# Kernel optimization log

Measured on AMD Instinct MI355X. Metric: run time of the kernel, lower is better.

Reference implementation:

```python
import jax, jax.numpy as jnp
import numpy as np

DIM_IN = 1024
DIM_OUT = 1024
B = 8192


def setup_inputs() -> dict:
    key = jax.random.key(0)
    ks = jax.random.split(key, 8)
    d = DIM_IN + DIM_OUT
    bound = 1.0 / np.sqrt(d)
    def lin(kw, kb):
        W = jax.random.uniform(kw, (d, DIM_OUT), jnp.float32, -bound, bound)
        b = jax.random.uniform(kb, (DIM_OUT,), jnp.float32, -bound, bound)
        return W, b
    kx, kh, kc, kp = ks[0], ks[1], ks[2], ks[3]
    pw = jax.random.split(kp, 8)
    W_I, b_I = lin(pw[0], pw[1])
    W_F, b_F = lin(pw[2], pw[3])
    W_G, b_G = lin(pw[4], pw[5])
    W_O, b_O = lin(pw[6], pw[7])
    return {
        "x": jax.random.normal(kx, (B, DIM_IN), jnp.float32),
        "h": jax.random.normal(kh, (B, DIM_OUT), jnp.float32),
        "c": jax.random.normal(kc, (B, DIM_OUT), jnp.float32),
        "W_I": W_I, "b_I": b_I,
        "W_F": W_F, "b_F": b_F,
        "W_G": W_G, "b_G": b_G,
        "W_O": W_O, "b_O": b_O,
    }


def reference(x, h, c, W_I, b_I, W_F, b_F, W_G, b_G, W_O, b_O):
    X = jnp.concatenate([x, h], axis=-1)  # [B, dimIn+dimOut]
    # Fuse the 4 gate projections into one GEMM: [B,d] @ [d, 4*dimOut]
    W = jnp.concatenate([W_I, W_F, W_G, W_O], axis=1)
    b = jnp.concatenate([b_I, b_F, b_G, b_O], axis=0)
    gates = X @ W + b
    i_, f_, g_, o_ = jnp.split(gates, 4, axis=-1)
    I = jax.nn.sigmoid(i_)
    F = jax.nn.sigmoid(f_)
    G = jnp.tanh(g_)
    O = jax.nn.sigmoid(o_)
    C = F * c + I * G
    return O * jnp.tanh(C), C
```

## Files before the change

### kernel.cpp

```cpp
#include <hip/hip_runtime.h>
#include <cstdint>


#define B_ROWS 8192
#define DK 2048
#define DOUT 1024
#define BM 256
#define BN 256
#define BK 64
#define NKT (DK / BK)

typedef __bf16 bf16x8 __attribute__((ext_vector_type(8)));
typedef __bf16 bf16x4 __attribute__((ext_vector_type(4)));
typedef float f32x4 __attribute__((ext_vector_type(4)));

__device__ inline void load16_to_lds(const __bf16* gsrc, __bf16* ldst) {
    __builtin_amdgcn_global_load_lds(
        (const __attribute__((address_space(1))) void*)gsrc,
        (__attribute__((address_space(3))) void*)ldst,
        16, 0, 0);
}

__device__ inline float fast_sigmoid(float x) {
    return __builtin_amdgcn_rcpf(1.0f + __builtin_amdgcn_exp2f(-1.442695041f * x));
}
__device__ inline float fast_tanh(float x) {
    return 1.0f - 2.0f * __builtin_amdgcn_rcpf(1.0f + __builtin_amdgcn_exp2f(2.885390082f * x));
}

__global__ __launch_bounds__(256) void prep_x(const float* __restrict__ x,
                                              const float* __restrict__ h,
                                              __bf16* __restrict__ X) {
    int id = blockIdx.x * 256 + threadIdx.x;
    int b = id >> 9;
    int k = (id & 511) * 4;
    float4 v;
    if (k < 1024) v = *(const float4*)&x[(size_t)b * 1024 + k];
    else          v = *(const float4*)&h[(size_t)b * 1024 + (k - 1024)];
    bf16x4 o = { (__bf16)v.x, (__bf16)v.y, (__bf16)v.z, (__bf16)v.w };
    *(bf16x4*)&X[(size_t)b * 2048 + k] = o;
}

__global__ __launch_bounds__(256) void prep_w(const float* __restrict__ WI,
                                              const float* __restrict__ WF,
                                              const float* __restrict__ WG,
                                              const float* __restrict__ WO,
                                              __bf16* __restrict__ Wt) {
    int kb = blockIdx.x;
    int jb = blockIdx.y;
    int j0 = jb * 32;
    __shared__ float t[32][33];
    int tx = threadIdx.x, ty = threadIdx.y;
    const float* Ws[4] = {WI, WF, WG, WO};
#pragma unroll
    for (int g = 0; g < 4; ++g) {
        const float* W = Ws[g];
#pragma unroll
        for (int yy = 0; yy < 32; yy += 8) {
            int k = kb * 32 + ty + yy;
            t[ty + yy][tx] = W[(size_t)k * 1024 + j0 + tx];
        }
        __syncthreads();
#pragma unroll
        for (int yy = 0; yy < 32; yy += 8) {
            int r = ty + yy;
            int npp = (jb * 2 + (r >> 4)) * 64 + g * 16 + (r & 15);
            Wt[(size_t)npp * 2048 + kb * 32 + tx] = (__bf16)t[tx][r];
        }
        __syncthreads();
    }
}

__global__ __launch_bounds__(512, 2) void lstm_gemm(
    const __bf16* __restrict__ Xbf, const __bf16* __restrict__ Wt,
    const float* __restrict__ c,
    const float* __restrict__ bI, const float* __restrict__ bF,
    const float* __restrict__ bG, const float* __restrict__ bO,
    float* __restrict__ outH, float* __restrict__ outC)
{
    __shared__ __bf16 lds[2][2][2][8192];

    const int tid  = threadIdx.x;
    const int lane = tid & 63;
    const int wave = tid >> 6;
    const int wm = wave >> 2;
    const int wn = wave & 3;

    const int bid = blockIdx.x;
    const int id  = (bid & 7) * 64 + (bid >> 3);
    const int mb = id & 31;
    const int nb = id >> 5;
    const int m0 = mb * BM;
    const int n0 = nb * BN;

    const int o0  = wave * 1024 + lane * 16;
    const int r0  = o0 >> 6;
    const int lc0 = ((o0 >> 4) & 3) ^ ((r0 >> 1) & 3);
    const __bf16* gA0 = Xbf + (size_t)(m0 + r0)       * DK + lc0 * 8;
    const __bf16* gA1 = Xbf + (size_t)(m0 + r0 + 128) * DK + lc0 * 8;
    const __bf16* gB0 = Wt  + (size_t)(n0 + r0)       * DK + lc0 * 8;
    const __bf16* gB1 = Wt  + (size_t)(n0 + r0 + 128) * DK + lc0 * 8;
    const int ls0 = wave * 512;
    const int ls1 = ls0 + 4096;

    const int lr = lane & 15;
    const int pc = (lane >> 4) ^ ((lr >> 1) & 3);
    const int ae = (wm * 128 + lr) * 32 + pc * 8;
    const int be = (wn * 64  + lr) * 32 + pc * 8;

    f32x4 acc[8][4];
#pragma unroll
    for (int i = 0; i < 8; ++i)
#pragma unroll
        for (int g = 0; g < 4; ++g) acc[i][g] = (f32x4){0.f, 0.f, 0.f, 0.f};

#define STAGE_A(d_, kh_, ko_) do { \
    load16_to_lds(gA0 + (ko_) + (kh_) * 32, &lds[d_][0][kh_][ls0]); \
    load16_to_lds(gA1 + (ko_) + (kh_) * 32, &lds[d_][0][kh_][ls1]); } while (0)
#define STAGE_B(d_, kh_, ko_) do { \
    load16_to_lds(gB0 + (ko_) + (kh_) * 32, &lds[d_][1][kh_][ls0]); \
    load16_to_lds(gB1 + (ko_) + (kh_) * 32, &lds[d_][1][kh_][ls1]); } while (0)

    STAGE_A(0, 0, 0);
    STAGE_B(0, 0, 0);
    STAGE_A(0, 1, 0);
    STAGE_B(0, 1, 0);

#pragma unroll 2
    for (int t = 0; t < NKT; ++t) {
        const int d  = t & 1;
        const int dn = d ^ 1;
        const int ko = ((t + 1) & (NKT - 1)) * BK;
#pragma unroll
        for (int kh = 0; kh < 2; ++kh) {
            asm volatile("s_waitcnt vmcnt(4) lgkmcnt(0)" ::: "memory");
            __builtin_amdgcn_s_barrier();
            asm volatile("" ::: "memory");
            bf16x8 a[8], b0, b1;
#pragma unroll
            for (int mi = 0; mi < 8; ++mi)
                a[mi] = *(const bf16x8*)&lds[d][0][kh][ae + mi * 512];
            b0 = *(const bf16x8*)&lds[d][1][kh][be];
            b1 = *(const bf16x8*)&lds[d][1][kh][be + 512];
            STAGE_A(dn, kh, ko);
            __builtin_amdgcn_s_setprio(1);
#pragma unroll
            for (int mi = 0; mi < 8; ++mi) {
                acc[mi][0] = __builtin_amdgcn_mfma_f32_16x16x32_bf16(a[mi], b0, acc[mi][0], 0, 0, 0);
                acc[mi][1] = __builtin_amdgcn_mfma_f32_16x16x32_bf16(a[mi], b1, acc[mi][1], 0, 0, 0);
            }
            __builtin_amdgcn_s_setprio(0);

            asm volatile("s_waitcnt lgkmcnt(0)" ::: "memory");
            __builtin_amdgcn_s_barrier();
            asm volatile("" ::: "memory");
            bf16x8 b2 = *(const bf16x8*)&lds[d][1][kh][be + 1024];
            bf16x8 b3 = *(const bf16x8*)&lds[d][1][kh][be + 1536];
            STAGE_B(dn, kh, ko);
            __builtin_amdgcn_s_setprio(1);
#pragma unroll
            for (int mi = 0; mi < 8; ++mi) {
                acc[mi][2] = __builtin_amdgcn_mfma_f32_16x16x32_bf16(a[mi], b2, acc[mi][2], 0, 0, 0);
                acc[mi][3] = __builtin_amdgcn_mfma_f32_16x16x32_bf16(a[mi], b3, acc[mi][3], 0, 0, 0);
            }
            __builtin_amdgcn_s_setprio(0);
        }
    }
#undef STAGE_A
#undef STAGE_B

    const int col = lane & 15;
    const int j = (nb * 4 + wn) * 16 + col;
    const float biI = bI[j], biF = bF[j], biG = bG[j], biO = bO[j];
    const int rbase = m0 + wm * 128 + ((lane >> 4) << 2);
#pragma unroll
    for (int mi = 0; mi < 8; ++mi) {
#pragma unroll
        for (int r = 0; r < 4; ++r) {
            int row = rbase + mi * 16 + r;
            float I = fast_sigmoid(acc[mi][0][r] + biI);
            float F = fast_sigmoid(acc[mi][1][r] + biF);
            float G = fast_tanh(acc[mi][2][r] + biG);
            float O = fast_sigmoid(acc[mi][3][r] + biO);
            size_t idx = (size_t)row * DOUT + j;
            float Cn = F * c[idx] + I * G;
            outH[idx] = O * fast_tanh(Cn);
            outC[idx] = Cn;
        }
    }
}

extern "C" void kernel_launch(void* const* d_in, const int* in_sizes, int n_in,
                              void* d_out, int out_size, void* d_ws, size_t ws_size,
                              hipStream_t stream) {
    const float* x  = (const float*)d_in[0];
    const float* h  = (const float*)d_in[1];
    const float* c  = (const float*)d_in[2];
    const float* WI = (const float*)d_in[3];
    const float* bI = (const float*)d_in[4];
    const float* WF = (const float*)d_in[5];
    const float* bF = (const float*)d_in[6];
    const float* WG = (const float*)d_in[7];
    const float* bG = (const float*)d_in[8];
    const float* WO = (const float*)d_in[9];
    const float* bO = (const float*)d_in[10];

    __bf16* Xbf = (__bf16*)d_ws;
    __bf16* Wt  = (__bf16*)((char*)d_ws + (size_t)B_ROWS * DK * 2);
    float* outH = (float*)d_out;
    float* outC = outH + (size_t)B_ROWS * DOUT;

    prep_x<<<(B_ROWS * DK / 4) / 256, 256, 0, stream>>>(x, h, Xbf);
    prep_w<<<dim3(DK / 32, DOUT / 32), dim3(32, 8), 0, stream>>>(WI, WF, WG, WO, Wt);
    lstm_gemm<<<dim3((B_ROWS / BM) * (4 * DOUT / BN)), dim3(512), 0, stream>>>(
        Xbf, Wt, c, bI, bF, bG, bO, outH, outC);
}
```

Measured before the change: 311.9 us.

## Switch GEMM to 32x32x16 MFMA with 4x2 wave layout and merge prep kernels

Replaces the 16x16x32 MFMA tiling with 32x32x16 MFMAs. Each wave now owns a 64x128 sub-tile instead of 128x64, which changes the LDS fragment offsets, the weight interleave order, and the epilogue row mapping to match. The K loop is manually unrolled into one load phase per 32-wide K half, with a single barrier instead of two and the A and B prefetches issued together, to cut LDS reads and barrier overhead. The two prep kernels are merged into one launch to remove a kernel launch. The risks are higher register pressure from the 16-wide accumulators and possible LDS bank conflicts in the new access pattern.

After: 312.2 us. About the same (+0.1%).

```diff
diff --git a/kernel.cpp b/kernel.cpp
--- a/kernel.cpp
+++ b/kernel.cpp
@@ -12,7 +12,7 @@
 
 typedef __bf16 bf16x8 __attribute__((ext_vector_type(8)));
 typedef __bf16 bf16x4 __attribute__((ext_vector_type(4)));
-typedef float f32x4 __attribute__((ext_vector_type(4)));
+typedef float f32x16 __attribute__((ext_vector_type(16)));
 
 __device__ inline void load16_to_lds(const __bf16* gsrc, __bf16* ldst) {
     __builtin_amdgcn_global_load_lds(
@@ -28,29 +28,29 @@
     return 1.0f - 2.0f * __builtin_amdgcn_rcpf(1.0f + __builtin_amdgcn_exp2f(2.885390082f * x));
 }
 
-__global__ __launch_bounds__(256) void prep_x(const float* __restrict__ x,
-                                              const float* __restrict__ h,
-                                              __bf16* __restrict__ X) {
-    int id = blockIdx.x * 256 + threadIdx.x;
-    int b = id >> 9;
-    int k = (id & 511) * 4;
-    float4 v;
-    if (k < 1024) v = *(const float4*)&x[(size_t)b * 1024 + k];
-    else          v = *(const float4*)&h[(size_t)b * 1024 + (k - 1024)];
-    bf16x4 o = { (__bf16)v.x, (__bf16)v.y, (__bf16)v.z, (__bf16)v.w };
-    *(bf16x4*)&X[(size_t)b * 2048 + k] = o;
-}
-
-__global__ __launch_bounds__(256) void prep_w(const float* __restrict__ WI,
-                                              const float* __restrict__ WF,
-                                              const float* __restrict__ WG,
-                                              const float* __restrict__ WO,
-                                              __bf16* __restrict__ Wt) {
-    int kb = blockIdx.x;
-    int jb = blockIdx.y;
+__global__ __launch_bounds__(256) void prep_all(
+    const float* __restrict__ x, const float* __restrict__ h,
+    __bf16* __restrict__ X,
+    const float* __restrict__ WI, const float* __restrict__ WF,
+    const float* __restrict__ WG, const float* __restrict__ WO,
+    __bf16* __restrict__ Wt)
+{
+    __shared__ float t[32][33];
+    if (blockIdx.x >= 2048) {
+        int id = (blockIdx.x - 2048) * 256 + threadIdx.x;
+        int b = id >> 9;
+        int k = (id & 511) * 4;
+        float4 v;
+        if (k < 1024) v = *(const float4*)&x[(size_t)b * 1024 + k];
+        else          v = *(const float4*)&h[(size_t)b * 1024 + (k - 1024)];
+        bf16x4 o = { (__bf16)v.x, (__bf16)v.y, (__bf16)v.z, (__bf16)v.w };
+        *(bf16x4*)&X[(size_t)b * 2048 + k] = o;
+        return;
+    }
+    int kb = blockIdx.x & 63;
+    int jb = blockIdx.x >> 6;
     int j0 = jb * 32;
-    __shared__ float t[32][33];
-    int tx = threadIdx.x, ty = threadIdx.y;
+    int tx = threadIdx.x & 31, ty = threadIdx.x >> 5;
     const float* Ws[4] = {WI, WF, WG, WO};
 #pragma unroll
     for (int g = 0; g < 4; ++g) {
@@ -64,7 +64,7 @@
 #pragma unroll
         for (int yy = 0; yy < 32; yy += 8) {
             int r = ty + yy;
-            int npp = (jb * 2 + (r >> 4)) * 64 + g * 16 + (r & 15);
+            int npp = jb * 128 + g * 32 + r;
             Wt[(size_t)npp * 2048 + kb * 32 + tx] = (__bf16)t[tx][r];
         }
         __syncthreads();
@@ -83,8 +83,8 @@
     const int tid  = threadIdx.x;
     const int lane = tid & 63;
     const int wave = tid >> 6;
-    const int wm = wave >> 2;
-    const int wn = wave & 3;
+    const int wm = wave >> 1;
+    const int wn = wave & 1;
 
     const int bid = blockIdx.x;
     const int id  = (bid & 7) * 64 + (bid >> 3);
@@ -103,16 +103,35 @@
     const int ls0 = wave * 512;
     const int ls1 = ls0 + 4096;
 
-    const int lr = lane & 15;
-    const int pc = (lane >> 4) ^ ((lr >> 1) & 3);
-    const int ae = (wm * 128 + lr) * 32 + pc * 8;
-    const int be = (wn * 64  + lr) * 32 + pc * 8;
-
-    f32x4 acc[8][4];
-#pragma unroll
-    for (int i = 0; i < 8; ++i)
-#pragma unroll
-        for (int g = 0; g < 4; ++g) acc[i][g] = (f32x4){0.f, 0.f, 0.f, 0.f};
+    const int lr = lane & 31;
+    const int kq = lane >> 5;
+    int aoff[2][2], boff[4][2];
+#pragma unroll
+    for (int mi = 0; mi < 2; ++mi) {
+        int row = wm * 64 + mi * 32 + lr;
+#pragma unroll
+        for (int ks = 0; ks < 2; ++ks) {
+            int pc = (kq + ks * 2) ^ ((row >> 1) & 3);
+            aoff[mi][ks] = row * 32 + pc * 8;
+        }
+    }
+#pragma unroll
+    for (int nf = 0; nf < 4; ++nf) {
+        int row = wn * 128 + nf * 32 + lr;
+#pragma unroll
+        for (int ks = 0; ks < 2; ++ks) {
+            int pc = (kq + ks * 2) ^ ((row >> 1) & 3);
+            boff[nf][ks] = row * 32 + pc * 8;
+        }
+    }
+
+    f32x16 acc[2][4];
+#pragma unroll
+    for (int mi = 0; mi < 2; ++mi)
+#pragma unroll
+        for (int nf = 0; nf < 4; ++nf)
+#pragma unroll
+            for (int e = 0; e < 16; ++e) acc[mi][nf][e] = 0.f;
 
 #define STAGE_A(d_, kh_, ko_) do { \
     load16_to_lds(gA0 + (ko_) + (kh_) * 32, &lds[d_][0][kh_][ls0]); \
@@ -121,67 +140,77 @@
     load16_to_lds(gB0 + (ko_) + (kh_) * 32, &lds[d_][1][kh_][ls0]); \
     load16_to_lds(gB1 + (ko_) + (kh_) * 32, &lds[d_][1][kh_][ls1]); } while (0)
 
+#define PHASE(d_, dn_, kh_, ko_, vm_, st_) do { \
+    asm volatile("s_waitcnt " vm_ " lgkmcnt(0)" ::: "memory"); \
+    __builtin_amdgcn_s_barrier(); \
+    asm volatile("" ::: "memory"); \
+    bf16x8 a0_  = *(const bf16x8*)&lds[d_][0][kh_][aoff[0][0]]; \
+    bf16x8 b0_  = *(const bf16x8*)&lds[d_][1][kh_][boff[0][0]]; \
+    bf16x8 b1_  = *(const bf16x8*)&lds[d_][1][kh_][boff[1][0]]; \
+    bf16x8 b2_  = *(const bf16x8*)&lds[d_][1][kh_][boff[2][0]]; \
+    bf16x8 b3_  = *(const bf16x8*)&lds[d_][1][kh_][boff[3][0]]; \
+    bf16x8 a1_  = *(const bf16x8*)&lds[d_][0][kh_][aoff[1][0]]; \
+    bf16x8 a0k_ = *(const bf16x8*)&lds[d_][0][kh_][aoff[0][1]]; \
+    bf16x8 b0k_ = *(const bf16x8*)&lds[d_][1][kh_][boff[0][1]]; \
+    bf16x8 b1k_ = *(const bf16x8*)&lds[d_][1][kh_][boff[1][1]]; \
+    bf16x8 b2k_ = *(const bf16x8*)&lds[d_][1][kh_][boff[2][1]]; \
+    bf16x8 b3k_ = *(const bf16x8*)&lds[d_][1][kh_][boff[3][1]]; \
+    bf16x8 a1k_ = *(const bf16x8*)&lds[d_][0][kh_][aoff[1][1]]; \
+    if (st_) { STAGE_A(dn_, kh_, ko_); STAGE_B(dn_, kh_, ko_); } \
+    __builtin_amdgcn_s_setprio(1); \
+    acc[0][0] = __builtin_amdgcn_mfma_f32_32x32x16_bf16(a0_, b0_, acc[0][0], 0, 0, 0); \
+    acc[0][1] = __builtin_amdgcn_mfma_f32_32x32x16_bf16(a0_, b1_, acc[0][1], 0, 0, 0); \
+    acc[0][2] = __builtin_amdgcn_mfma_f32_32x32x16_bf16(a0_, b2_, acc[0][2], 0, 0, 0); \
+    acc[0][3] = __builtin_amdgcn_mfma_f32_32x32x16_bf16(a0_, b3_, acc[0][3], 0, 0, 0); \
+    acc[1][0] = __builtin_amdgcn_mfma_f32_32x32x16_bf16(a1_, b0_, acc[1][0], 0, 0, 0); \
+    acc[1][1] = __builtin_amdgcn_mfma_f32_32x32x16_bf16(a1_, b1_, acc[1][1], 0, 0, 0); \
+    acc[1][2] = __builtin_amdgcn_mfma_f32_32x32x16_bf16(a1_, b2_, acc[1][2], 0, 0, 0); \
+    acc[1][3] = __builtin_amdgcn_mfma_f32_32x32x16_bf16(a1_, b3_, acc[1][3], 0, 0, 0); \
+    acc[0][0] = __builtin_amdgcn_mfma_f32_32x32x16_bf16(a0k_, b0k_, acc[0][0], 0, 0, 0); \
+    acc[0][1] = __builtin_amdgcn_mfma_f32_32x32x16_bf16(a0k_, b1k_, acc[0][1], 0, 0, 0); \
+    acc[0][2] = __builtin_amdgcn_mfma_f32_32x32x16_bf16(a0k_, b2k_, acc[0][2], 0, 0, 0); \
+    acc[0][3] = __builtin_amdgcn_mfma_f32_32x32x16_bf16(a0k_, b3k_, acc[0][3], 0, 0, 0); \
+    acc[1][0] = __builtin_amdgcn_mfma_f32_32x32x16_bf16(a1k_, b0k_, acc[1][0], 0, 0, 0); \
+    acc[1][1] = __builtin_amdgcn_mfma_f32_32x32x16_bf16(a1k_, b1k_, acc[1][1], 0, 0, 0); \
+    acc[1][2] = __builtin_amdgcn_mfma_f32_32x32x16_bf16(a1k_, b2k_, acc[1][2], 0, 0, 0); \
+    acc[1][3] = __builtin_amdgcn_mfma_f32_32x32x16_bf16(a1k_, b3k_, acc[1][3], 0, 0, 0); \
+    __builtin_amdgcn_s_setprio(0); \
+} while (0)
+
     STAGE_A(0, 0, 0);
     STAGE_B(0, 0, 0);
     STAGE_A(0, 1, 0);
     STAGE_B(0, 1, 0);
 
-#pragma unroll 2
-    for (int t = 0; t < NKT; ++t) {
-        const int d  = t & 1;
-        const int dn = d ^ 1;
-        const int ko = ((t + 1) & (NKT - 1)) * BK;
-#pragma unroll
-        for (int kh = 0; kh < 2; ++kh) {
-            asm volatile("s_waitcnt vmcnt(4) lgkmcnt(0)" ::: "memory");
-            __builtin_amdgcn_s_barrier();
-            asm volatile("" ::: "memory");
-            bf16x8 a[8], b0, b1;
-#pragma unroll
-            for (int mi = 0; mi < 8; ++mi)
-                a[mi] = *(const bf16x8*)&lds[d][0][kh][ae + mi * 512];
-            b0 = *(const bf16x8*)&lds[d][1][kh][be];
-            b1 = *(const bf16x8*)&lds[d][1][kh][be + 512];
-            STAGE_A(dn, kh, ko);
-            __builtin_amdgcn_s_setprio(1);
-#pragma unroll
-            for (int mi = 0; mi < 8; ++mi) {
-                acc[mi][0] = __builtin_amdgcn_mfma_f32_16x16x32_bf16(a[mi], b0, acc[mi][0], 0, 0, 0);
-                acc[mi][1] = __builtin_amdgcn_mfma_f32_16x16x32_bf16(a[mi], b1, acc[mi][1], 0, 0, 0);
-            }
-            __builtin_amdgcn_s_setprio(0);
-
-            asm volatile("s_waitcnt lgkmcnt(0)" ::: "memory");
-            __builtin_amdgcn_s_barrier();
-            asm volatile("" ::: "memory");
-            bf16x8 b2 = *(const bf16x8*)&lds[d][1][kh][be + 1024];
-            bf16x8 b3 = *(const bf16x8*)&lds[d][1][kh][be + 1536];
-            STAGE_B(dn, kh, ko);
-            __builtin_amdgcn_s_setprio(1);
-#pragma unroll
-            for (int mi = 0; mi < 8; ++mi) {
-                acc[mi][2] = __builtin_amdgcn_mfma_f32_16x16x32_bf16(a[mi], b2, acc[mi][2], 0, 0, 0);
-                acc[mi][3] = __builtin_amdgcn_mfma_f32_16x16x32_bf16(a[mi], b3, acc[mi][3], 0, 0, 0);
-            }
-            __builtin_amdgcn_s_setprio(0);
-        }
-    }
+    for (int t = 0; t < NKT - 2; t += 2) {
+        const int ko0 = (t + 1) * BK;
+        const int ko1 = (t + 2) * BK;
+        PHASE(0, 1, 0, ko0, "vmcnt(4)", 1);
+        PHASE(0, 1, 1, ko0, "vmcnt(4)", 1);
+        PHASE(1, 0, 0, ko1, "vmcnt(4)", 1);
+        PHASE(1, 0, 1, ko1, "vmcnt(4)", 1);
+    }
+    PHASE(0, 1, 0, (NKT - 1) * BK, "vmcnt(4)", 1);
+    PHASE(0, 1, 1, (NKT - 1) * BK, "vmcnt(4)", 1);
+    PHASE(1, 0, 0, 0, "vmcnt(4)", 0);
+    PHASE(1, 0, 1, 0, "vmcnt(0)", 0);
+
+#undef PHASE
 #undef STAGE_A
 #undef STAGE_B
 
-    const int col = lane & 15;
-    const int j = (nb * 4 + wn) * 16 + col;
+    const int j = (nb * 2 + wn) * 32 + lr;
     const float biI = bI[j], biF = bF[j], biG = bG[j], biO = bO[j];
-    const int rbase = m0 + wm * 128 + ((lane >> 4) << 2);
-#pragma unroll
-    for (int mi = 0; mi < 8; ++mi) {
-#pragma unroll
-        for (int r = 0; r < 4; ++r) {
-            int row = rbase + mi * 16 + r;
-            float I = fast_sigmoid(acc[mi][0][r] + biI);
-            float F = fast_sigmoid(acc[mi][1][r] + biF);
-            float G = fast_tanh(acc[mi][2][r] + biG);
-            float O = fast_sigmoid(acc[mi][3][r] + biO);
+    const int rb = m0 + wm * 64 + 4 * kq;
+#pragma unroll
+    for (int mi = 0; mi < 2; ++mi) {
+#pragma unroll
+        for (int rg = 0; rg < 16; ++rg) {
+            int row = rb + mi * 32 + (rg & 3) + 8 * (rg >> 2);
+            float I = fast_sigmoid(acc[mi][0][rg] + biI);
+            float F = fast_sigmoid(acc[mi][1][rg] + biF);
+            float G = fast_tanh(acc[mi][2][rg] + biG);
+            float O = fast_sigmoid(acc[mi][3][rg] + biO);
             size_t idx = (size_t)row * DOUT + j;
             float Cn = F * c[idx] + I * G;
             outH[idx] = O * fast_tanh(Cn);
@@ -210,8 +239,8 @@
     float* outH = (float*)d_out;
     float* outC = outH + (size_t)B_ROWS * DOUT;
 
-    prep_x<<<(B_ROWS * DK / 4) / 256, 256, 0, stream>>>(x, h, Xbf);
-    prep_w<<<dim3(DK / 32, DOUT / 32), dim3(32, 8), 0, stream>>>(WI, WF, WG, WO, Wt);
+    prep_all<<<2048 + (B_ROWS * DK / 4) / 256, 256, 0, stream>>>(
+        x, h, Xbf, WI, WF, WG, WO, Wt);
     lstm_gemm<<<dim3((B_ROWS / BM) * (4 * DOUT / BN)), dim3(512), 0, stream>>>(
         Xbf, Wt, c, bI, bF, bG, bO, outH, outC);
 }
```
